# Kernel optimization log

Hardware: AMD Instinct MI355X
Metric: run time of the kernel (lower is better)

## Reference

```python
import jax, jax.numpy as jnp
import numpy as np

D = 1024            # text/user embedding length
HID = 3 * D         # 2*text_D + user_D = MLP hidden width
OUT = 8             # output_shape (int)


def setup_inputs() -> dict:
    key = jax.random.key(0)
    ks = jax.random.split(key, 9)
    T, U = 256, 128
    s = 1.0 / np.sqrt(HID)
    return {
        "text_a": jax.random.normal(ks[0], (T, D), jnp.float32),
        "text_b": jax.random.normal(ks[1], (T, D), jnp.float32),
        "user_embeddings": jax.random.normal(ks[2], (U, D), jnp.float32),
        "W1": jax.random.uniform(ks[3], (HID, HID), jnp.float32, -s, s),
        "b1": jax.random.uniform(ks[4], (HID,), jnp.float32, -s, s),
        "W2": jax.random.uniform(ks[5], (HID, HID), jnp.float32, -s, s),
        "b2": jax.random.uniform(ks[6], (HID,), jnp.float32, -s, s),
        "W3": jax.random.uniform(ks[7], (OUT, HID), jnp.float32, -s, s),
        "b3": jax.random.uniform(ks[8], (OUT,), jnp.float32, -s, s),
    }


def reference(text_a, text_b, user_embeddings, W1, b1, W2, b2, W3, b3):
    # min/max over the set of text embedding tensors
    t_min = jnp.minimum(text_a, text_b)          # (T, D)
    t_max = jnp.maximum(text_a, text_b)          # (T, D)
    T, U = t_min.shape[0], user_embeddings.shape[0]
    # combined[t, u] = concat(t_min[t], t_max[t], user[u])  -> (T, U, 3D)
    text_part = jnp.broadcast_to(
        jnp.concatenate([t_min, t_max], axis=-1)[:, None, :], (T, U, 2 * D))
    user_part = jnp.broadcast_to(user_embeddings[None, :, :], (T, U, D))
    x = jnp.concatenate([text_part, user_part], axis=-1)  # (T, U, 3D)
    # 3-layer MLP (no activation, no dropout by default)
    x = jnp.einsum('tuh,oh->tuo', x, W1) + b1
    x = jnp.einsum('tuh,oh->tuo', x, W2) + b2
    x = jnp.einsum('tuh,oh->tuo', x, W3) + b3
    return x  # (T, U, OUT)
```

## Files before the change

### kernel.cpp

```cpp
#include <hip/hip_runtime.h>
#include <hip/hip_bf16.h>


#define HIDN 3072
#define DIM 1024
#define NOUT 8
#define NS 32
#define KPS 96
#define WK 24
#define GX 12
#define TDIM 256
#define UDIM 128

__device__ __forceinline__ float dot4(float4 a, float4 b) {
    return a.x * b.x + a.y * b.y + a.z * b.z + a.w * b.w;
}
__device__ __forceinline__ float4 add4(float4 a, float4 b) {
    return make_float4(a.x + b.x, a.y + b.y, a.z + b.z, a.w + b.w);
}

__device__ __forceinline__ void bias_slice_fold(const float* As,
                                                const float* __restrict__ bvec,
                                                float* __restrict__ cp,
                                                int s, int tid) {
    const int o = tid >> 5, k5 = tid & 31;
    float acc = 0.f;
#pragma unroll
    for (int j = 0; j < KPS / 32; ++j)
        acc += As[o * KPS + k5 + 32 * j] * bvec[s * KPS + k5 + 32 * j];
#pragma unroll
    for (int off = 16; off; off >>= 1) acc += __shfl_down(acc, off, 32);
    if (k5 == 0) cp[s * NOUT + o] = acc;
}

__global__ __launch_bounds__(256) void gemm_partial(
    const float* __restrict__ A_rows, const float* __restrict__ part_in,
    const float* __restrict__ B, float* __restrict__ part_out,
    const float* __restrict__ bvec, float* __restrict__ cp, int mode) {
    const int s = blockIdx.y, gx = blockIdx.x;
    const int tid = threadIdx.x;
    const int lane = tid & 63, w = tid >> 6;

    __shared__ float As[NOUT * KPS];
    __shared__ float4 red[4 * NOUT * 64];

    if (mode == 0) {
        for (int i = tid; i < NOUT * KPS; i += 256)
            As[i] = A_rows[(i / KPS) * HIDN + s * KPS + (i % KPS)];
    } else {
        for (int j4 = tid; j4 < NOUT * KPS / 4; j4 += 256) {
            const int o = j4 / (KPS / 4), kk4 = j4 % (KPS / 4);
            const float4* pp = (const float4*)(part_in + (size_t)o * HIDN
                                               + s * KPS) + kk4;
            float4 a = make_float4(0.f, 0.f, 0.f, 0.f);
#pragma unroll 8
            for (int sp = 0; sp < NS; ++sp)
                a = add4(a, pp[(size_t)sp * (NOUT * HIDN / 4)]);
            ((float4*)As)[j4] = a;
        }
    }
    __syncthreads();
    if (gx == 0) bias_slice_fold(As, bvec, cp, s, tid);

    const int h = gx * 256 + lane * 4;
    const int k0 = s * KPS + w * WK;
    const float4* Bp = (const float4*)(B + (size_t)k0 * HIDN) + (h >> 2);

    float4 bv[WK];
#pragma unroll
    for (int kk = 0; kk < WK; ++kk) bv[kk] = Bp[(size_t)kk * (HIDN / 4)];

    float4 acc[NOUT];
#pragma unroll
    for (int o = 0; o < NOUT; ++o) acc[o] = make_float4(0.f, 0.f, 0.f, 0.f);
#pragma unroll
    for (int kk = 0; kk < WK; ++kk) {
#pragma unroll
        for (int o = 0; o < NOUT; ++o) {
            float a = As[o * KPS + w * WK + kk];
            acc[o].x += a * bv[kk].x; acc[o].y += a * bv[kk].y;
            acc[o].z += a * bv[kk].z; acc[o].w += a * bv[kk].w;
        }
    }

#pragma unroll
    for (int o = 0; o < NOUT; ++o) red[(w * NOUT + o) * 64 + lane] = acc[o];
    __syncthreads();
#pragma unroll
    for (int j = 0; j < 2; ++j) {
        const int o = w * 2 + j;
        float4 r = add4(add4(red[(0 * NOUT + o) * 64 + lane],
                             red[(1 * NOUT + o) * 64 + lane]),
                        add4(red[(2 * NOUT + o) * 64 + lane],
                             red[(3 * NOUT + o) * 64 + lane]));
        *(float4*)(part_out + ((size_t)s * NOUT + o) * HIDN + h) = r;
    }
}

__global__ __launch_bounds__(256) void mid_kernel(const float* __restrict__ part2,
                                                  const float* __restrict__ user,
                                                  float* __restrict__ Mt,
                                                  float* __restrict__ Qpart) {
    const int b = blockIdx.x, tid = threadIdx.x;
    const float4* p4 = (const float4*)part2;

    if (b < 16) {
        const int i4 = b * 256 + tid;
        const int o = i4 >> 9, j4 = i4 & 511;
        float4 a = make_float4(0.f, 0.f, 0.f, 0.f);
#pragma unroll 8
        for (int s = 0; s < NS; ++s)
            a = add4(a, p4[((size_t)s * NOUT + o) * (HIDN / 4) + j4]);
        ((float4*)Mt)[o * 512 + j4] = a;
        return;
    }

    const int dg = b - 16;
    __shared__ float4 Mu4[NOUT * 32];
    {
        const int o = tid >> 5, j4 = tid & 31;
        float4 a = make_float4(0.f, 0.f, 0.f, 0.f);
#pragma unroll 8
        for (int s = 0; s < NS; ++s)
            a = add4(a, p4[((size_t)s * NOUT + o) * (HIDN / 4) + 512 + dg * 32 + j4]);
        Mu4[o * 32 + j4] = a;
    }
    __syncthreads();

    const int u = tid >> 1, o0 = (tid & 1) * 4;
    const float4* uv = (const float4*)(user) + u * (DIM / 4) + dg * 32;
    float q[4] = {0.f, 0.f, 0.f, 0.f};
    for (int j = 0; j < 32; ++j) {
        float4 x = uv[j];
#pragma unroll
        for (int oo = 0; oo < 4; ++oo)
            q[oo] += dot4(Mu4[(o0 + oo) * 32 + j], x);
    }
    *(float4*)(Qpart + ((size_t)dg * UDIM + u) * NOUT + o0) =
        make_float4(q[0], q[1], q[2], q[3]);
}

__global__ __launch_bounds__(256) void out_kernel(
    const float* __restrict__ ta, const float* __restrict__ tb,
    const float* __restrict__ Mt, const float* __restrict__ Qpart,
    const float* __restrict__ cp1, const float* __restrict__ cp2,
    const float* __restrict__ b3, float4* __restrict__ out) {
    const int t = blockIdx.x, tid = threadIdx.x;
    const int lane = tid & 63, w = tid >> 6;

    const float4* Mt4 = (const float4*)Mt;
    float4 a = ((const float4*)ta)[t * (DIM / 4) + tid];
    float4 b = ((const float4*)tb)[t * (DIM / 4) + tid];
    float4 mn = make_float4(fminf(a.x, b.x), fminf(a.y, b.y),
                            fminf(a.z, b.z), fminf(a.w, b.w));
    float4 mx = make_float4(fmaxf(a.x, b.x), fmaxf(a.y, b.y),
                            fmaxf(a.z, b.z), fmaxf(a.w, b.w));
    float acc[NOUT];
#pragma unroll
    for (int o = 0; o < NOUT; ++o) {
        float4 ml = Mt4[o * 512 + tid];
        float4 mh = Mt4[o * 512 + 256 + tid];
        acc[o] = dot4(ml, mn) + dot4(mh, mx);
    }
#pragma unroll
    for (int o = 0; o < NOUT; ++o) {
#pragma unroll
        for (int off = 32; off > 0; off >>= 1)
            acc[o] += __shfl_down(acc[o], off, 64);
    }
    __shared__ float red[4][NOUT];
    __shared__ float c8[NOUT];
    if (lane == 0) {
#pragma unroll
        for (int o = 0; o < NOUT; ++o) red[w][o] = acc[o];
    }

    const int u = tid >> 1, half = tid & 1;
    const float4* Qp4 = (const float4*)Qpart;
    float4 q = make_float4(0.f, 0.f, 0.f, 0.f);
#pragma unroll
    for (int dg = 0; dg < 8; ++dg)
        q = add4(q, Qp4[((size_t)dg * UDIM + u) * 2 + half]);

    if (tid < NOUT) {
        float cc = b3[tid];
#pragma unroll 8
        for (int s = 0; s < NS; ++s)
            cc += cp1[s * NOUT + tid] + cp2[s * NOUT + tid];
        c8[tid] = cc;
    }
    __syncthreads();

    const int o0 = half * 4;
    float4 pv = make_float4(
        red[0][o0 + 0] + red[1][o0 + 0] + red[2][o0 + 0] + red[3][o0 + 0],
        red[0][o0 + 1] + red[1][o0 + 1] + red[2][o0 + 1] + red[3][o0 + 1],
        red[0][o0 + 2] + red[1][o0 + 2] + red[2][o0 + 2] + red[3][o0 + 2],
        red[0][o0 + 3] + red[1][o0 + 3] + red[2][o0 + 3] + red[3][o0 + 3]);
    float4 cv = make_float4(c8[o0], c8[o0 + 1], c8[o0 + 2], c8[o0 + 3]);
    out[(size_t)t * 256 + tid] = add4(add4(pv, q), cv);
}

extern "C" void kernel_launch(void* const* d_in, const int* in_sizes, int n_in,
                              void* d_out, int out_size, void* d_ws, size_t ws_size,
                              hipStream_t stream) {
    const float* text_a = (const float*)d_in[0];
    const float* text_b = (const float*)d_in[1];
    const float* user   = (const float*)d_in[2];
    const float* W1 = (const float*)d_in[3];
    const float* b1 = (const float*)d_in[4];
    const float* W2 = (const float*)d_in[5];
    const float* b2 = (const float*)d_in[6];
    const float* W3 = (const float*)d_in[7];
    const float* b3 = (const float*)d_in[8];

    float* ws = (float*)d_ws;
    float* part1 = ws;
    float* part2 = part1 + (size_t)NS * NOUT * HIDN;
    float* Mt    = part2 + (size_t)NS * NOUT * HIDN;
    float* Qpart = Mt + NOUT * 2048;
    float* cp1   = Qpart + 8 * UDIM * NOUT;
    float* cp2   = cp1 + NS * NOUT;

    gemm_partial<<<dim3(GX, NS), 256, 0, stream>>>(W3, nullptr, W2, part1,
                                                   b2, cp2, 0);
    gemm_partial<<<dim3(GX, NS), 256, 0, stream>>>(nullptr, part1, W1, part2,
                                                   b1, cp1, 1);
    mid_kernel<<<24, 256, 0, stream>>>(part2, user, Mt, Qpart);
    out_kernel<<<TDIM, 256, 0, stream>>>(text_a, text_b, Mt, Qpart,
                                         cp1, cp2, b3, (float4*)d_out);
}
```

Measured before the change: 36.93 us.

## Fuse mid reduction into second GEMM via atomics, drop a kernel launch

The separate mid_kernel, which summed 32 split-K partials and projected user embeddings, is removed. The second GEMM now accumulates its per-slice results straight into Mt with float atomics. Blocks covering the user columns compute the user projection on the spot and atomically add it into Q. Zeroing of Mt and Q moves into the first GEMM kernel. This saves one launch and the partial-buffer round trip, at the cost of many atomic adds and a non-deterministic summation order.

```diff
diff --git a/kernel.cpp b/kernel.cpp
--- a/kernel.cpp
+++ b/kernel.cpp
@@ -12,11 +12,12 @@
 #define TDIM 256
 #define UDIM 128
 
+__device__ __forceinline__ float4 f4z() { return make_float4(0.f, 0.f, 0.f, 0.f); }
+__device__ __forceinline__ float4 add4(float4 a, float4 b) {
+    return make_float4(a.x + b.x, a.y + b.y, a.z + b.z, a.w + b.w);
+}
 __device__ __forceinline__ float dot4(float4 a, float4 b) {
     return a.x * b.x + a.y * b.y + a.z * b.z + a.w * b.w;
-}
-__device__ __forceinline__ float4 add4(float4 a, float4 b) {
-    return make_float4(a.x + b.x, a.y + b.y, a.z + b.z, a.w + b.w);
 }
 
 __device__ __forceinline__ void bias_slice_fold(const float* As,
@@ -33,46 +34,17 @@
     if (k5 == 0) cp[s * NOUT + o] = acc;
 }
 
-__global__ __launch_bounds__(256) void gemm_partial(
-    const float* __restrict__ A_rows, const float* __restrict__ part_in,
-    const float* __restrict__ B, float* __restrict__ part_out,
-    const float* __restrict__ bvec, float* __restrict__ cp, int mode) {
-    const int s = blockIdx.y, gx = blockIdx.x;
-    const int tid = threadIdx.x;
-    const int lane = tid & 63, w = tid >> 6;
-
-    __shared__ float As[NOUT * KPS];
-    __shared__ float4 red[4 * NOUT * 64];
-
-    if (mode == 0) {
-        for (int i = tid; i < NOUT * KPS; i += 256)
-            As[i] = A_rows[(i / KPS) * HIDN + s * KPS + (i % KPS)];
-    } else {
-        for (int j4 = tid; j4 < NOUT * KPS / 4; j4 += 256) {
-            const int o = j4 / (KPS / 4), kk4 = j4 % (KPS / 4);
-            const float4* pp = (const float4*)(part_in + (size_t)o * HIDN
-                                               + s * KPS) + kk4;
-            float4 a = make_float4(0.f, 0.f, 0.f, 0.f);
-#pragma unroll 8
-            for (int sp = 0; sp < NS; ++sp)
-                a = add4(a, pp[(size_t)sp * (NOUT * HIDN / 4)]);
-            ((float4*)As)[j4] = a;
-        }
-    }
-    __syncthreads();
-    if (gx == 0) bias_slice_fold(As, bvec, cp, s, tid);
-
+__device__ __forceinline__ void gemm_core(const float* __restrict__ B,
+                                          const float* As, int s, int gx,
+                                          int lane, int w, float4 acc[NOUT]) {
     const int h = gx * 256 + lane * 4;
     const int k0 = s * KPS + w * WK;
     const float4* Bp = (const float4*)(B + (size_t)k0 * HIDN) + (h >> 2);
-
     float4 bv[WK];
 #pragma unroll
     for (int kk = 0; kk < WK; ++kk) bv[kk] = Bp[(size_t)kk * (HIDN / 4)];
-
-    float4 acc[NOUT];
-#pragma unroll
-    for (int o = 0; o < NOUT; ++o) acc[o] = make_float4(0.f, 0.f, 0.f, 0.f);
+#pragma unroll
+    for (int o = 0; o < NOUT; ++o) acc[o] = f4z();
 #pragma unroll
     for (int kk = 0; kk < WK; ++kk) {
 #pragma unroll
@@ -82,10 +54,38 @@
             acc[o].z += a * bv[kk].z; acc[o].w += a * bv[kk].w;
         }
     }
+}
+
+__global__ __launch_bounds__(256) void k1_gemm(
+    const float* __restrict__ W3, const float* __restrict__ W2,
+    const float* __restrict__ b2, float* __restrict__ part1,
+    float* __restrict__ cp2, float* __restrict__ Mt, float* __restrict__ Q) {
+    const int s = blockIdx.y, gx = blockIdx.x;
+    const int tid = threadIdx.x;
+    const int lane = tid & 63, w = tid >> 6;
+
+    const int bid = s * GX + gx;
+    if (bid < 256) {
+        if (tid < 64) Mt[bid * 64 + tid] = 0.f;
+    } else if (bid < 272) {
+        if (tid < 64) Q[(bid - 256) * 64 + tid] = 0.f;
+    }
+
+    __shared__ float As[NOUT * KPS];
+    __shared__ float4 red[4 * NOUT * 64];
+
+    for (int i = tid; i < NOUT * KPS; i += 256)
+        As[i] = W3[(i / KPS) * HIDN + s * KPS + (i % KPS)];
+    __syncthreads();
+    if (gx == 0) bias_slice_fold(As, b2, cp2, s, tid);
+
+    float4 acc[NOUT];
+    gemm_core(W2, As, s, gx, lane, w, acc);
 
 #pragma unroll
     for (int o = 0; o < NOUT; ++o) red[(w * NOUT + o) * 64 + lane] = acc[o];
     __syncthreads();
+    const int h = gx * 256 + lane * 4;
 #pragma unroll
     for (int j = 0; j < 2; ++j) {
         const int o = w * 2 + j;
@@ -93,64 +93,94 @@
                              red[(1 * NOUT + o) * 64 + lane]),
                         add4(red[(2 * NOUT + o) * 64 + lane],
                              red[(3 * NOUT + o) * 64 + lane]));
-        *(float4*)(part_out + ((size_t)s * NOUT + o) * HIDN + h) = r;
-    }
-}
-
-__global__ __launch_bounds__(256) void mid_kernel(const float* __restrict__ part2,
-                                                  const float* __restrict__ user,
-                                                  float* __restrict__ Mt,
-                                                  float* __restrict__ Qpart) {
-    const int b = blockIdx.x, tid = threadIdx.x;
-    const float4* p4 = (const float4*)part2;
-
-    if (b < 16) {
-        const int i4 = b * 256 + tid;
-        const int o = i4 >> 9, j4 = i4 & 511;
-        float4 a = make_float4(0.f, 0.f, 0.f, 0.f);
+        *(float4*)(part1 + ((size_t)s * NOUT + o) * HIDN + h) = r;
+    }
+}
+
+__global__ __launch_bounds__(256) void k2_gemm(
+    const float* __restrict__ part1, const float* __restrict__ W1,
+    const float* __restrict__ user, const float* __restrict__ b1,
+    float* __restrict__ cp1, float* __restrict__ Mt, float* __restrict__ Q) {
+    const int s = blockIdx.y, gx = blockIdx.x;
+    const int tid = threadIdx.x;
+    const int lane = tid & 63, w = tid >> 6;
+
+    __shared__ float As[NOUT * KPS];
+    __shared__ float4 red[4 * NOUT * 64];
+    __shared__ float4 Mu4[NOUT * 64];
+
+    for (int j4 = tid; j4 < NOUT * KPS / 4; j4 += 256) {
+        const int o = j4 / (KPS / 4), kk4 = j4 % (KPS / 4);
+        const float4* pp = (const float4*)(part1 + (size_t)o * HIDN
+                                           + s * KPS) + kk4;
+        float4 a = f4z();
 #pragma unroll 8
-        for (int s = 0; s < NS; ++s)
-            a = add4(a, p4[((size_t)s * NOUT + o) * (HIDN / 4) + j4]);
-        ((float4*)Mt)[o * 512 + j4] = a;
-        return;
-    }
-
-    const int dg = b - 16;
-    __shared__ float4 Mu4[NOUT * 32];
-    {
-        const int o = tid >> 5, j4 = tid & 31;
-        float4 a = make_float4(0.f, 0.f, 0.f, 0.f);
-#pragma unroll 8
-        for (int s = 0; s < NS; ++s)
-            a = add4(a, p4[((size_t)s * NOUT + o) * (HIDN / 4) + 512 + dg * 32 + j4]);
-        Mu4[o * 32 + j4] = a;
-    }
-    __syncthreads();
-
-    const int u = tid >> 1, o0 = (tid & 1) * 4;
-    const float4* uv = (const float4*)(user) + u * (DIM / 4) + dg * 32;
-    float q[4] = {0.f, 0.f, 0.f, 0.f};
-    for (int j = 0; j < 32; ++j) {
-        float4 x = uv[j];
+        for (int sp = 0; sp < NS; ++sp)
+            a = add4(a, pp[(size_t)sp * (NOUT * HIDN / 4)]);
+        ((float4*)As)[j4] = a;
+    }
+    __syncthreads();
+    if (gx == 0) bias_slice_fold(As, b1, cp1, s, tid);
+
+    float4 acc[NOUT];
+    gemm_core(W1, As, s, gx, lane, w, acc);
+
+#pragma unroll
+    for (int o = 0; o < NOUT; ++o) red[(w * NOUT + o) * 64 + lane] = acc[o];
+    __syncthreads();
+
+    if (gx < 8) {
+        const int h = gx * 256 + lane * 4;
+#pragma unroll
+        for (int j = 0; j < 2; ++j) {
+            const int o = w * 2 + j;
+            float4 r = add4(add4(red[(0 * NOUT + o) * 64 + lane],
+                                 red[(1 * NOUT + o) * 64 + lane]),
+                            add4(red[(2 * NOUT + o) * 64 + lane],
+                                 red[(3 * NOUT + o) * 64 + lane]));
+            float* dst = Mt + o * 2048 + h;
+            unsafeAtomicAdd(dst + 0, r.x);
+            unsafeAtomicAdd(dst + 1, r.y);
+            unsafeAtomicAdd(dst + 2, r.z);
+            unsafeAtomicAdd(dst + 3, r.w);
+        }
+    } else {
+#pragma unroll
+        for (int j = 0; j < 2; ++j) {
+            const int o = w * 2 + j;
+            Mu4[o * 64 + lane] = add4(add4(red[(0 * NOUT + o) * 64 + lane],
+                                           red[(1 * NOUT + o) * 64 + lane]),
+                                      add4(red[(2 * NOUT + o) * 64 + lane],
+                                           red[(3 * NOUT + o) * 64 + lane]));
+        }
+        __syncthreads();
+        const int u = tid >> 1, o0 = (tid & 1) * 4;
+        const float4* uv = (const float4*)user + (size_t)u * (DIM / 4)
+                           + (gx - 8) * 64;
+        float q[4] = {0.f, 0.f, 0.f, 0.f};
+        for (int j = 0; j < 64; ++j) {
+            float4 x = uv[j];
+#pragma unroll
+            for (int oo = 0; oo < 4; ++oo)
+                q[oo] += dot4(Mu4[(o0 + oo) * 64 + j], x);
+        }
 #pragma unroll
         for (int oo = 0; oo < 4; ++oo)
-            q[oo] += dot4(Mu4[(o0 + oo) * 32 + j], x);
-    }
-    *(float4*)(Qpart + ((size_t)dg * UDIM + u) * NOUT + o0) =
-        make_float4(q[0], q[1], q[2], q[3]);
-}
-
-__global__ __launch_bounds__(256) void out_kernel(
+            unsafeAtomicAdd(Q + u * NOUT + o0 + oo, q[oo]);
+    }
+}
+
+__global__ __launch_bounds__(256) void k3_out(
     const float* __restrict__ ta, const float* __restrict__ tb,
-    const float* __restrict__ Mt, const float* __restrict__ Qpart,
+    const float* __restrict__ Mt, const float* __restrict__ Q,
     const float* __restrict__ cp1, const float* __restrict__ cp2,
     const float* __restrict__ b3, float4* __restrict__ out) {
     const int t = blockIdx.x, tid = threadIdx.x;
     const int lane = tid & 63, w = tid >> 6;
 
     const float4* Mt4 = (const float4*)Mt;
-    float4 a = ((const float4*)ta)[t * (DIM / 4) + tid];
-    float4 b = ((const float4*)tb)[t * (DIM / 4) + tid];
+    float4 a = ((const float4*)ta)[(size_t)t * (DIM / 4) + tid];
+    float4 b = ((const float4*)tb)[(size_t)t * (DIM / 4) + tid];
     float4 mn = make_float4(fminf(a.x, b.x), fminf(a.y, b.y),
                             fminf(a.z, b.z), fminf(a.w, b.w));
     float4 mx = make_float4(fmaxf(a.x, b.x), fmaxf(a.y, b.y),
@@ -174,14 +204,6 @@
 #pragma unroll
         for (int o = 0; o < NOUT; ++o) red[w][o] = acc[o];
     }
-
-    const int u = tid >> 1, half = tid & 1;
-    const float4* Qp4 = (const float4*)Qpart;
-    float4 q = make_float4(0.f, 0.f, 0.f, 0.f);
-#pragma unroll
-    for (int dg = 0; dg < 8; ++dg)
-        q = add4(q, Qp4[((size_t)dg * UDIM + u) * 2 + half]);
-
     if (tid < NOUT) {
         float cc = b3[tid];
 #pragma unroll 8
@@ -191,7 +213,8 @@
     }
     __syncthreads();
 
-    const int o0 = half * 4;
+    const int u = tid >> 1, half = tid & 1, o0 = half * 4;
+    float4 q = ((const float4*)Q)[u * 2 + half];
     float4 pv = make_float4(
         red[0][o0 + 0] + red[1][o0 + 0] + red[2][o0 + 0] + red[3][o0 + 0],
         red[0][o0 + 1] + red[1][o0 + 1] + red[2][o0 + 1] + red[3][o0 + 1],
@@ -216,17 +239,13 @@
 
     float* ws = (float*)d_ws;
     float* part1 = ws;
-    float* part2 = part1 + (size_t)NS * NOUT * HIDN;
-    float* Mt    = part2 + (size_t)NS * NOUT * HIDN;
-    float* Qpart = Mt + NOUT * 2048;
-    float* cp1   = Qpart + 8 * UDIM * NOUT;
+    float* Mt    = part1 + (size_t)NS * NOUT * HIDN;
+    float* Q     = Mt + NOUT * 2048;
+    float* cp1   = Q + UDIM * NOUT;
     float* cp2   = cp1 + NS * NOUT;
 
-    gemm_partial<<<dim3(GX, NS), 256, 0, stream>>>(W3, nullptr, W2, part1,
-                                                   b2, cp2, 0);
-    gemm_partial<<<dim3(GX, NS), 256, 0, stream>>>(nullptr, part1, W1, part2,
-                                                   b1, cp1, 1);
-    mid_kernel<<<24, 256, 0, stream>>>(part2, user, Mt, Qpart);
-    out_kernel<<<TDIM, 256, 0, stream>>>(text_a, text_b, Mt, Qpart,
-                                         cp1, cp2, b3, (float4*)d_out);
-}
+    k1_gemm<<<dim3(GX, NS), 256, 0, stream>>>(W3, W2, b2, part1, cp2, Mt, Q);
+    k2_gemm<<<dim3(GX, NS), 256, 0, stream>>>(part1, W1, user, b1, cp1, Mt, Q);
+    k3_out<<<TDIM, 256, 0, stream>>>(text_a, text_b, Mt, Q, cp1, cp2, b3,
+                                     (float4*)d_out);
+}
```

Measured after the change: 46.74 us. 26.6% more time.

## Spread mid-stage split-K reduction over more blocks and hoist bias fold

Applied to the files above, without the earlier changes.

The mid kernel grows from 24 to 97 blocks. Each block now reduces the 32 split-K partials with four waves summing 8 slices each, combined through shared memory. The user-projection stage is split into 32 finer chunks instead of 8, and the user slice is loaded into registers. The constant bias fold (b3 plus the cp1/cp2 partials) moves from every output block into one extra mid block. The aim is to shorten the latency-bound serial reduction in the mid stage, at the cost of the output kernel summing 32 Q partials per element instead of 8.

```diff
diff --git a/kernel.cpp b/kernel.cpp
--- a/kernel.cpp
+++ b/kernel.cpp
@@ -11,12 +11,14 @@
 #define GX 12
 #define TDIM 256
 #define UDIM 128
-
+#define PF4 6144
+
+__device__ __forceinline__ float4 f4z() { return make_float4(0.f, 0.f, 0.f, 0.f); }
+__device__ __forceinline__ float4 add4(float4 a, float4 b) {
+    return make_float4(a.x + b.x, a.y + b.y, a.z + b.z, a.w + b.w);
+}
 __device__ __forceinline__ float dot4(float4 a, float4 b) {
     return a.x * b.x + a.y * b.y + a.z * b.z + a.w * b.w;
-}
-__device__ __forceinline__ float4 add4(float4 a, float4 b) {
-    return make_float4(a.x + b.x, a.y + b.y, a.z + b.z, a.w + b.w);
 }
 
 __device__ __forceinline__ void bias_slice_fold(const float* As,
@@ -52,10 +54,10 @@
             const int o = j4 / (KPS / 4), kk4 = j4 % (KPS / 4);
             const float4* pp = (const float4*)(part_in + (size_t)o * HIDN
                                                + s * KPS) + kk4;
-            float4 a = make_float4(0.f, 0.f, 0.f, 0.f);
+            float4 a = f4z();
 #pragma unroll 8
             for (int sp = 0; sp < NS; ++sp)
-                a = add4(a, pp[(size_t)sp * (NOUT * HIDN / 4)]);
+                a = add4(a, pp[(size_t)sp * PF4]);
             ((float4*)As)[j4] = a;
         }
     }
@@ -72,7 +74,7 @@
 
     float4 acc[NOUT];
 #pragma unroll
-    for (int o = 0; o < NOUT; ++o) acc[o] = make_float4(0.f, 0.f, 0.f, 0.f);
+    for (int o = 0; o < NOUT; ++o) acc[o] = f4z();
 #pragma unroll
     for (int kk = 0; kk < WK; ++kk) {
 #pragma unroll
@@ -97,60 +99,87 @@
     }
 }
 
-__global__ __launch_bounds__(256) void mid_kernel(const float* __restrict__ part2,
-                                                  const float* __restrict__ user,
-                                                  float* __restrict__ Mt,
-                                                  float* __restrict__ Qpart) {
+__global__ __launch_bounds__(256) void k3_mid(
+    const float* __restrict__ part2, const float* __restrict__ user,
+    const float* __restrict__ cp1, const float* __restrict__ cp2,
+    const float* __restrict__ b3, float* __restrict__ Mt,
+    float* __restrict__ Qpart, float* __restrict__ cvec) {
     const int b = blockIdx.x, tid = threadIdx.x;
     const float4* p4 = (const float4*)part2;
 
-    if (b < 16) {
-        const int i4 = b * 256 + tid;
-        const int o = i4 >> 9, j4 = i4 & 511;
-        float4 a = make_float4(0.f, 0.f, 0.f, 0.f);
+    if (b < 64) {
+        const int lane = tid & 63, w = tid >> 6;
+        const int i4 = b * 64 + lane;
+        const int o = i4 >> 9, h4 = i4 & 511;
+        float4 acc = f4z();
+#pragma unroll
+        for (int j = 0; j < 8; ++j)
+            acc = add4(acc, p4[(size_t)(w * 8 + j) * PF4 + o * 768 + h4]);
+        __shared__ float4 red2[4 * 64];
+        red2[w * 64 + lane] = acc;
+        __syncthreads();
+        if (w == 0) {
+            float4 r = add4(add4(red2[lane], red2[64 + lane]),
+                            add4(red2[128 + lane], red2[192 + lane]));
+            ((float4*)Mt)[i4] = r;
+        }
+        return;
+    }
+
+    if (b < 96) {
+        const int ub = b - 64;
+        __shared__ float4 mup[4 * 64];
+        __shared__ float4 Mu4[NOUT * 8];
+        const int tgt = tid & 63, grp = tid >> 6;
+        const int o = tgt >> 3, j4 = tgt & 7;
+        float4 a = f4z();
+#pragma unroll
+        for (int j = 0; j < 8; ++j)
+            a = add4(a, p4[(size_t)(grp * 8 + j) * PF4 + o * 768 + 512 + ub * 8 + j4]);
+        mup[grp * 64 + tgt] = a;
+        __syncthreads();
+        if (tid < 64)
+            Mu4[tid] = add4(add4(mup[tid], mup[64 + tid]),
+                            add4(mup[128 + tid], mup[192 + tid]));
+        __syncthreads();
+
+        const int u = tid >> 1, o0 = (tid & 1) * 4;
+        const float4* uv = (const float4*)user + (size_t)u * (DIM / 4) + ub * 8;
+        float4 x8[8];
+#pragma unroll
+        for (int j = 0; j < 8; ++j) x8[j] = uv[j];
+        float q[4];
+#pragma unroll
+        for (int oo = 0; oo < 4; ++oo) {
+            float s = 0.f;
+#pragma unroll
+            for (int j = 0; j < 8; ++j) s += dot4(Mu4[(o0 + oo) * 8 + j], x8[j]);
+            q[oo] = s;
+        }
+        ((float4*)Qpart)[((size_t)ub * UDIM + (tid >> 1)) * 2 + (tid & 1)] =
+            make_float4(q[0], q[1], q[2], q[3]);
+        return;
+    }
+
+    if (tid < NOUT) {
+        float cc = b3[tid];
 #pragma unroll 8
         for (int s = 0; s < NS; ++s)
-            a = add4(a, p4[((size_t)s * NOUT + o) * (HIDN / 4) + j4]);
-        ((float4*)Mt)[o * 512 + j4] = a;
-        return;
-    }
-
-    const int dg = b - 16;
-    __shared__ float4 Mu4[NOUT * 32];
-    {
-        const int o = tid >> 5, j4 = tid & 31;
-        float4 a = make_float4(0.f, 0.f, 0.f, 0.f);
-#pragma unroll 8
-        for (int s = 0; s < NS; ++s)
-            a = add4(a, p4[((size_t)s * NOUT + o) * (HIDN / 4) + 512 + dg * 32 + j4]);
-        Mu4[o * 32 + j4] = a;
-    }
-    __syncthreads();
-
-    const int u = tid >> 1, o0 = (tid & 1) * 4;
-    const float4* uv = (const float4*)(user) + u * (DIM / 4) + dg * 32;
-    float q[4] = {0.f, 0.f, 0.f, 0.f};
-    for (int j = 0; j < 32; ++j) {
-        float4 x = uv[j];
-#pragma unroll
-        for (int oo = 0; oo < 4; ++oo)
-            q[oo] += dot4(Mu4[(o0 + oo) * 32 + j], x);
-    }
-    *(float4*)(Qpart + ((size_t)dg * UDIM + u) * NOUT + o0) =
-        make_float4(q[0], q[1], q[2], q[3]);
-}
-
-__global__ __launch_bounds__(256) void out_kernel(
+            cc += cp1[s * NOUT + tid] + cp2[s * NOUT + tid];
+        cvec[tid] = cc;
+    }
+}
+
+__global__ __launch_bounds__(256) void k4_out(
     const float* __restrict__ ta, const float* __restrict__ tb,
     const float* __restrict__ Mt, const float* __restrict__ Qpart,
-    const float* __restrict__ cp1, const float* __restrict__ cp2,
-    const float* __restrict__ b3, float4* __restrict__ out) {
+    const float* __restrict__ cvec, float4* __restrict__ out) {
     const int t = blockIdx.x, tid = threadIdx.x;
     const int lane = tid & 63, w = tid >> 6;
 
     const float4* Mt4 = (const float4*)Mt;
-    float4 a = ((const float4*)ta)[t * (DIM / 4) + tid];
-    float4 b = ((const float4*)tb)[t * (DIM / 4) + tid];
+    float4 a = ((const float4*)ta)[(size_t)t * (DIM / 4) + tid];
+    float4 b = ((const float4*)tb)[(size_t)t * (DIM / 4) + tid];
     float4 mn = make_float4(fminf(a.x, b.x), fminf(a.y, b.y),
                             fminf(a.z, b.z), fminf(a.w, b.w));
     float4 mx = make_float4(fmaxf(a.x, b.x), fmaxf(a.y, b.y),
@@ -169,35 +198,25 @@
             acc[o] += __shfl_down(acc[o], off, 64);
     }
     __shared__ float red[4][NOUT];
-    __shared__ float c8[NOUT];
     if (lane == 0) {
 #pragma unroll
         for (int o = 0; o < NOUT; ++o) red[w][o] = acc[o];
     }
-
-    const int u = tid >> 1, half = tid & 1;
+    __syncthreads();
+
+    const int u = tid >> 1, half = tid & 1, o0 = half * 4;
     const float4* Qp4 = (const float4*)Qpart;
-    float4 q = make_float4(0.f, 0.f, 0.f, 0.f);
-#pragma unroll
-    for (int dg = 0; dg < 8; ++dg)
-        q = add4(q, Qp4[((size_t)dg * UDIM + u) * 2 + half]);
-
-    if (tid < NOUT) {
-        float cc = b3[tid];
+    float4 q = f4z();
 #pragma unroll 8
-        for (int s = 0; s < NS; ++s)
-            cc += cp1[s * NOUT + tid] + cp2[s * NOUT + tid];
-        c8[tid] = cc;
-    }
-    __syncthreads();
-
-    const int o0 = half * 4;
+    for (int ub = 0; ub < 32; ++ub)
+        q = add4(q, Qp4[((size_t)ub * UDIM + u) * 2 + half]);
+
+    float4 cv = ((const float4*)cvec)[half];
     float4 pv = make_float4(
         red[0][o0 + 0] + red[1][o0 + 0] + red[2][o0 + 0] + red[3][o0 + 0],
         red[0][o0 + 1] + red[1][o0 + 1] + red[2][o0 + 1] + red[3][o0 + 1],
         red[0][o0 + 2] + red[1][o0 + 2] + red[2][o0 + 2] + red[3][o0 + 2],
         red[0][o0 + 3] + red[1][o0 + 3] + red[2][o0 + 3] + red[3][o0 + 3]);
-    float4 cv = make_float4(c8[o0], c8[o0 + 1], c8[o0 + 2], c8[o0 + 3]);
     out[(size_t)t * 256 + tid] = add4(add4(pv, q), cv);
 }
 
@@ -219,14 +238,15 @@
     float* part2 = part1 + (size_t)NS * NOUT * HIDN;
     float* Mt    = part2 + (size_t)NS * NOUT * HIDN;
     float* Qpart = Mt + NOUT * 2048;
-    float* cp1   = Qpart + 8 * UDIM * NOUT;
+    float* cp1   = Qpart + 32 * UDIM * NOUT;
     float* cp2   = cp1 + NS * NOUT;
+    float* cvec  = cp2 + NS * NOUT;
 
     gemm_partial<<<dim3(GX, NS), 256, 0, stream>>>(W3, nullptr, W2, part1,
                                                    b2, cp2, 0);
     gemm_partial<<<dim3(GX, NS), 256, 0, stream>>>(nullptr, part1, W1, part2,
                                                    b1, cp1, 1);
-    mid_kernel<<<24, 256, 0, stream>>>(part2, user, Mt, Qpart);
-    out_kernel<<<TDIM, 256, 0, stream>>>(text_a, text_b, Mt, Qpart,
-                                         cp1, cp2, b3, (float4*)d_out);
-}
+    k3_mid<<<97, 256, 0, stream>>>(part2, user, cp1, cp2, b3, Mt, Qpart, cvec);
+    k4_out<<<TDIM, 256, 0, stream>>>(text_a, text_b, Mt, Qpart, cvec,
+                                     (float4*)d_out);
+}
```

New measurement: 33.79 us. 1.09x faster.
